# Performance work log

Measured on AMD Instinct MI355X. Metric: run time of the kernel, lower is better.

Reference implementation:

```python
import jax, jax.numpy as jnp
import numpy as np

B, T, D = 2, 4096, 1024
HD, HQ, KVH, W = 128, 8, 1, 1024   # head_dim, q_heads, kv_heads, window
HH, HG, K = 1536, 2048, 4          # hawk hidden, gmlp hidden, conv kernel
ALPHA_SCALE = float(np.log(8.0))   # alpha_log_scale (stored as log, used exp'd)


def setup_inputs() -> dict:
    key = jax.random.key(0)
    ks = jax.random.split(key, 16)
    n = lambda k, shape, std: jax.random.normal(k, shape, jnp.float32) * std
    return {
        'x': n(ks[0], (B, T, D), 1.0),
        'sn_g': jnp.ones((D,), jnp.float32),
        'q_w': n(ks[1], (HQ * HD, D), D ** -0.5),
        'kv_w': n(ks[2], (2 * KVH * HD, D), D ** -0.5),
        'ao_w': n(ks[3], (D, D), D ** -0.5),
        'sgn_g': jnp.ones((D,), jnp.float32),
        'sg_grow': n(ks[4], (2 * HG, D), D ** -0.5),
        'sg_shrink': n(ks[5], (D, HG), HG ** -0.5),
        'hn_g': jnp.ones((D,), jnp.float32),
        'h_in_w': n(ks[6], (2 * HH, D), D ** -0.5),
        'h_conv_w': n(ks[7], (HH, 1, K), K ** -0.5),
        'h_conv_b': jnp.zeros((HH,), jnp.float32),
        'h_gates_w': n(ks[8], (2 * HH, HH), HH ** -0.5),
        'h_gates_b': jnp.zeros((2 * HH,), jnp.float32),
        'h_forget': jnp.linspace(-4.323, -9.0, HH, dtype=jnp.float32),
        'h_out_w': n(ks[9], (D, HH), HH ** -0.5),
        'hgn_g': jnp.ones((D,), jnp.float32),
        'hg_grow': n(ks[10], (2 * HG, D), D ** -0.5),
        'hg_shrink': n(ks[11], (D, HG), HG ** -0.5),
    }


def rmsnorm(x, gamma):
    # original: gamma / dim**-0.5 * x / ||x||_2  (no eps)
    inv = jax.lax.rsqrt(jnp.sum(x * x, axis=-1, keepdims=True))
    return gamma * (x.shape[-1] ** 0.5) * x * inv


def rope(x, base=10000.0):
    # x: (B, T, H, HD); interleaved rotary over time axis 1
    t = x.shape[1]
    hd = x.shape[-1]
    inv = 1.0 / (base ** (jnp.arange(0, hd, 2, dtype=jnp.float32) / hd))
    ang = jnp.arange(t, dtype=jnp.float32)[:, None] * inv[None, :]  # (T, HD/2)
    cos = jnp.cos(ang)[None, :, None, :]
    sin = jnp.sin(ang)[None, :, None, :]
    x1, x2 = x[..., 0::2], x[..., 1::2]
    y1 = x1 * cos - x2 * sin
    y2 = x1 * sin + x2 * cos
    return jnp.stack([y1, y2], axis=-1).reshape(x.shape)


def sliding_mqa(x, q_w, kv_w, ao_w):
    # MQA with causal sliding window of W, computed in blocks of W
    q = (x @ q_w.T).reshape(B, T, HQ, HD)
    kv = (x @ kv_w.T).reshape(B, T, 2, KVH, HD)
    k = kv[:, :, 0, 0]  # (B, T, HD) since KVH == 1
    v = kv[:, :, 1, 0]
    q = rope(q)
    k = rope(k[:, :, None, :])[:, :, 0]
    nb = T // W
    qb = q.reshape(B, nb, W, HQ, HD)
    kb = k.reshape(B, nb, W, HD)
    vb = v.reshape(B, nb, W, HD)
    # prepend previous block (zeros for block 0)
    shift = lambda a: jnp.concatenate([jnp.zeros_like(a[:, :1]), a[:, :-1]], axis=1)
    k2 = jnp.concatenate([shift(kb), kb], axis=2)  # (B, nb, 2W, HD)
    v2 = jnp.concatenate([shift(vb), vb], axis=2)
    qi = jnp.arange(W)[:, None]
    kj = jnp.arange(2 * W)[None, :]
    base = (kj >= qi) & (kj <= qi + W)  # causal + window (i-j <= W)
    blk0 = base & (kj >= W)             # block 0 has no real previous block
    mask = jnp.where(jnp.arange(nb)[:, None, None] == 0, blk0[None], base[None])
    scores = jnp.einsum('bnqhd,bnkd->bhnqk', qb, k2) * (HD ** -0.5)
    scores = jnp.where(mask[None, None], scores, -jnp.inf)
    p = jax.nn.softmax(scores, axis=-1)
    o = jnp.einsum('bhnqk,bnkd->bnqhd', p, v2).reshape(B, T, HQ * HD)
    return o @ ao_w.T


def gated_mlp(x, grow_w, shrink_w):
    gate, h = jnp.split(x @ grow_w.T, 2, axis=-1)
    return (jax.nn.gelu(gate, approximate=False) * h) @ shrink_w.T


def hawk(x, in_w, conv_w, conv_b, gates_w, gates_b, forget_base, out_w):
    gate, u = jnp.split(x @ in_w.T, 2, axis=-1)  # (B, T, HH) each
    # depthwise causal conv1d (torch pads k-1 both sides then slices [:T])
    u_nch = jnp.transpose(u, (0, 2, 1))  # (B, HH, T)
    c = jax.lax.conv_general_dilated(
        u_nch, conv_w, window_strides=(1,), padding=[(K - 1, 0)],
        feature_group_count=HH, dimension_numbers=('NCH', 'OIH', 'NCH'))
    xc = jnp.transpose(c + conv_b[None, :, None], (0, 2, 1))  # (B, T, HH)
    fg, ig = jnp.split(xc @ gates_w.T + gates_b, 2, axis=-1)
    log_alpha = -np.exp(ALPHA_SCALE) * jax.nn.softplus(forget_base) * jax.nn.sigmoid(fg)
    alpha = jnp.exp(log_alpha)
    beta = jnp.sqrt(1.0 - alpha * alpha + 1e-6)
    xin = beta * jax.nn.sigmoid(ig) * xc
    # linear recurrence h_t = alpha_t * h_{t-1} + xin_t  via associative scan
    def combine(c1, c2):
        a1, x1 = c1
        a2, x2 = c2
        return a1 * a2, a2 * x1 + x2
    _, h = jax.lax.associative_scan(combine, (alpha, xin), axis=1)
    return (jax.nn.gelu(gate, approximate=False) * h) @ out_w.T


def reference(x, sn_g, q_w, kv_w, ao_w, sgn_g, sg_grow, sg_shrink,
              hn_g, h_in_w, h_conv_w, h_conv_b, h_gates_w, h_gates_b,
              h_forget, h_out_w, hgn_g, hg_grow, hg_shrink):
    x = x + sliding_mqa(rmsnorm(x, sn_g), q_w, kv_w, ao_w)
    x = x + gated_mlp(rmsnorm(x, sgn_g), sg_grow, sg_shrink)
    x = x + hawk(rmsnorm(x, hn_g), h_in_w, h_conv_w, h_conv_b,
                 h_gates_w, h_gates_b, h_forget, h_out_w)
    x = x + gated_mlp(rmsnorm(x, hgn_g), hg_grow, hg_shrink)
    return x
```

## Files before the change

### kernel.cpp

```cpp
#include <hip/hip_runtime.h>
#include <hip/hip_bf16.h>
#include <math.h>

#define B_  2
#define T_  4096
#define D_  1024
#define HD_ 128
#define HQ_ 8
#define W_  1024
#define HH_ 1536
#define HG_ 2048
#define KC_ 4

typedef float  f32x4  __attribute__((ext_vector_type(4)));
typedef float  f32x2  __attribute__((ext_vector_type(2)));
typedef __bf16 bf16x8 __attribute__((ext_vector_type(8)));
typedef unsigned short u16;
typedef unsigned short u16x2 __attribute__((ext_vector_type(2)));
typedef unsigned short u16x4 __attribute__((ext_vector_type(4)));
typedef unsigned short u16x8 __attribute__((ext_vector_type(8)));

__device__ __forceinline__ u16 f2bf(float f) {
    unsigned int u = __builtin_bit_cast(unsigned int, f);
    u += 0x7fffu + ((u >> 16) & 1u);
    return (u16)(u >> 16);
}
__device__ __forceinline__ float bf2f(u16 v) {
    unsigned int u = ((unsigned int)v) << 16;
    return __builtin_bit_cast(float, u);
}
__device__ __forceinline__ float gelu_exact(float x) {
    return 0.5f * x * (1.0f + erff(x * 0.70710678118654752f));
}
__device__ __forceinline__ float sigmoidf_(float x) {
    return 1.0f / (1.0f + expf(-x));
}

#define GLOAD16(gp, lp) __builtin_amdgcn_global_load_lds( \
    (const __attribute__((address_space(1))) void*)(gp),  \
    (__attribute__((address_space(3))) void*)(lp), 16, 0, 0)

__global__ void cvt_kernel(const float* __restrict__ src, u16* __restrict__ dst, long n)
{
    long i = ((long)blockIdx.x * blockDim.x + threadIdx.x) * 8;
    if (i >= n) return;
    f32x4 a = *(const f32x4*)(src + i);
    f32x4 b = *(const f32x4*)(src + i + 4);
    u16x4 ua, ub;
    ua.x = f2bf(a.x); ua.y = f2bf(a.y); ua.z = f2bf(a.z); ua.w = f2bf(a.w);
    ub.x = f2bf(b.x); ub.y = f2bf(b.y); ub.z = f2bf(b.z); ub.w = f2bf(b.w);
    *(u16x4*)(dst + i) = ua;
    *(u16x4*)(dst + i + 4) = ub;
}

template<int EPI, bool OBF>
__global__ __launch_bounds__(256)
void gemm_bf16_kernel(const u16* __restrict__ A, const u16* __restrict__ Bw,
                      const float* __restrict__ bias, const float* __restrict__ res,
                      const u16* gatebuf, void* outv,
                      int M, int N, int K)
{
    __shared__ u16 lA[2][128 * 32];
    __shared__ u16 lB[2][128 * 32];
    const int n0 = blockIdx.x * 128, m0 = blockIdx.y * 128;
    const int tid = threadIdx.x, w = tid >> 6, l = tid & 63;
    const int wr = w >> 1, wc = w & 1, lr = l & 15, lg = l >> 4;

    f32x4 acc[4][4];
#pragma unroll
    for (int i = 0; i < 4; i++)
#pragma unroll
        for (int j = 0; j < 4; j++) acc[i][j] = {0.f, 0.f, 0.f, 0.f};

    const int srow = w * 16 + (l >> 2);
    const int gslot = ((l & 3) - ((l >> 3) & 3)) & 3;
    const u16* gA = A + (long)(m0 + srow) * K + gslot * 8;
    const u16* gB = Bw + (long)(n0 + srow) * K + gslot * 8;
    const int lofs = w * 512 + l * 8;

#define STAGE_G(buf, kk)                                        \
    {                                                           \
        GLOAD16(gA + (kk),              &lA[buf][lofs]);        \
        GLOAD16(gA + (long)64 * K + (kk), &lA[buf][2048 + lofs]); \
        GLOAD16(gB + (kk),              &lB[buf][lofs]);        \
        GLOAD16(gB + (long)64 * K + (kk), &lB[buf][2048 + lofs]); \
    }

    STAGE_G(0, 0);
    __syncthreads();

    const int NT = K >> 5;
    const int swzr = (lr >> 1) & 3;
    for (int t = 0; t < NT; ++t) {
        const int cur = t & 1;
        if (t + 1 < NT) STAGE_G(cur ^ 1, (t + 1) << 5);
        bf16x8 af[4], bfr[4];
#pragma unroll
        for (int m = 0; m < 4; m++)
            af[m] = *(const bf16x8*)&lA[cur][(wr * 64 + m * 16 + lr) * 32 + (((lg + swzr) & 3) * 8)];
#pragma unroll
        for (int n = 0; n < 4; n++)
            bfr[n] = *(const bf16x8*)&lB[cur][(wc * 64 + n * 16 + lr) * 32 + (((lg + swzr) & 3) * 8)];
#pragma unroll
        for (int m = 0; m < 4; m++)
#pragma unroll
            for (int n = 0; n < 4; n++)
                acc[m][n] = __builtin_amdgcn_mfma_f32_16x16x32_bf16(af[m], bfr[n], acc[m][n], 0, 0, 0);
        __syncthreads();
    }
#undef STAGE_G

#pragma unroll
    for (int m = 0; m < 4; m++)
#pragma unroll
        for (int n = 0; n < 4; n++) {
            const int col = n0 + wc * 64 + n * 16 + lr;
            const float bv = (EPI == 1) ? bias[col] : 0.f;
#pragma unroll
            for (int r = 0; r < 4; r++) {
                const int row = m0 + wr * 64 + m * 16 + lg * 4 + r;
                const long idx = (long)row * N + col;
                float v = acc[m][n][r] + bv;
                if (EPI == 2) v += res[idx];
                if (EPI == 3) v = gelu_exact(bf2f(gatebuf[idx])) * v;
                if (OBF) ((u16*)outv)[idx] = f2bf(v);
                else     ((float*)outv)[idx] = v;
            }
        }
}

__global__ __launch_bounds__(256)
void rmsnorm_kernel(const float* __restrict__ x, const float* __restrict__ g,
                    u16* __restrict__ out)
{
    const long row = blockIdx.x;
    const int tid = threadIdx.x;
    const float* xp = x + row * D_;
    f32x4 v = *(const f32x4*)(xp + tid * 4);
    float ss = v.x * v.x + v.y * v.y + v.z * v.z + v.w * v.w;
#pragma unroll
    for (int o = 1; o < 64; o <<= 1) ss += __shfl_xor(ss, o);
    __shared__ float ps[4];
    if ((tid & 63) == 0) ps[tid >> 6] = ss;
    __syncthreads();
    float tot = ps[0] + ps[1] + ps[2] + ps[3];
    float inv = rsqrtf(tot) * 32.0f;
    f32x4 gv = *(const f32x4*)(g + tid * 4);
    u16x4 o4;
    o4.x = f2bf(gv.x * v.x * inv); o4.y = f2bf(gv.y * v.y * inv);
    o4.z = f2bf(gv.z * v.z * inv); o4.w = f2bf(gv.w * v.w * inv);
    *(u16x4*)(out + row * D_ + tid * 4) = o4;
}

__global__ void rope_bf16_kernel(const float* __restrict__ q, const float* __restrict__ kv,
                                 u16* __restrict__ qb, u16* __restrict__ kb)
{
    const long NQ = (long)B_ * T_ * HQ_ * 64;
    const long NK = (long)B_ * T_ * 64;
    long idx = (long)blockIdx.x * blockDim.x + threadIdx.x;
    if (idx >= NQ + NK) return;
    int i; long t; const float* src; u16* dst;
    if (idx < NQ) {
        i = idx & 63;
        long bth = idx >> 6;
        t = (bth / HQ_) % T_;
        src = q + bth * HD_ + 2 * i;
        dst = qb + bth * HD_ + 2 * i;
    } else {
        long k = idx - NQ;
        i = k & 63;
        long bt = k >> 6;
        t = bt % T_;
        src = kv + bt * (2 * HD_) + 2 * i;
        dst = kb + bt * HD_ + 2 * i;
    }
    float freq = exp2f(-(float)i * 0.20762050593046014f);
    float ang = (float)t * freq;
    float sn, cs;
    sincosf(ang, &sn, &cs);
    f32x2 xv = *(const f32x2*)src;
    u16x2 yv;
    yv.x = f2bf(xv.x * cs - xv.y * sn);
    yv.y = f2bf(xv.x * sn + xv.y * cs);
    *(u16x2*)dst = yv;
}

__global__ __launch_bounds__(256)
void vtrans_kernel(const float* __restrict__ kv, u16* __restrict__ vt)
{
    __shared__ float tile[64][65];
    const int t0 = blockIdx.x * 64, d0 = blockIdx.y * 64, b = blockIdx.z;
    const int tid = threadIdx.x;
    {
        const int tl = tid & 63, dg = tid >> 6;
        const float* vp = kv + (((long)b * T_ + t0 + tl) * 2 + 1) * HD_ + d0 + dg * 16;
#pragma unroll
        for (int j = 0; j < 4; j++) {
            f32x4 v = *(const f32x4*)(vp + j * 4);
            tile[dg * 16 + j * 4 + 0][tl] = v.x;
            tile[dg * 16 + j * 4 + 1][tl] = v.y;
            tile[dg * 16 + j * 4 + 2][tl] = v.z;
            tile[dg * 16 + j * 4 + 3][tl] = v.w;
        }
    }
    __syncthreads();
    {
        const int dl = tid >> 2, tg = (tid & 3) * 16;
        u16x8 a, c;
#pragma unroll
        for (int j = 0; j < 8; j++) a[j] = f2bf(tile[dl][tg + j]);
#pragma unroll
        for (int j = 0; j < 8; j++) c[j] = f2bf(tile[dl][tg + 8 + j]);
        u16* dst = vt + ((long)b * HD_ + d0 + dl) * T_ + t0 + tg;
        *(u16x8*)dst = a;
        *(u16x8*)(dst + 8) = c;
    }
}

#define PLD 72

__global__ __launch_bounds__(256)
void attn_mfma3_kernel(const u16* __restrict__ qb, const u16* __restrict__ kb,
                       const u16* __restrict__ vt, u16* __restrict__ o)
{
    __shared__ u16 Ksh[2][64 * 128];
    __shared__ u16 Vsh[2][128 * 64];
    __shared__ u16 Psh[4 * 16 * PLD];

    const int qt = blockIdx.x, h = blockIdx.y, b = blockIdx.z;
    const int q0 = qt * 64;
    const int tid = threadIdx.x;
    const int w = tid >> 6, l = tid & 63;
    const int lr = l & 15, lg = l >> 4;

    bf16x8 qfr[4];
    {
        const u16* qp = qb + (((long)b * T_ + q0 + w * 16 + lr) * HQ_ + h) * HD_;
#pragma unroll
        for (int kt = 0; kt < 4; kt++)
            qfr[kt] = *(const bf16x8*)(qp + kt * 32 + lg * 8);
    }

    int oK[4], oV[4];
#pragma unroll
    for (int i = 0; i < 4; i++) {
        int krow = w * 16 + i * 4 + (l >> 4);
        int kc8 = (l & 15) ^ (krow & 7);
        oK[i] = krow * 128 + kc8 * 8;
        int vrow = w * 32 + i * 8 + (l >> 3);
        int vc8 = (l & 7) ^ (vrow & 7);
        oV[i] = vrow * T_ + vc8 * 8;
    }
    const u16* kbase = kb + (long)b * T_ * HD_;
    const u16* vbase = vt + (long)b * HD_ * T_;

    f32x4 oacc[8];
#pragma unroll
    for (int dt = 0; dt < 8; dt++) oacc[dt] = {0.f, 0.f, 0.f, 0.f};
    float mrun[4], srun[4];
#pragma unroll
    for (int r = 0; r < 4; r++) { mrun[r] = -1e30f; srun[r] = 0.f; }

    const int kt_lo = (q0 >= W_) ? (q0 - W_) : 0;
    const int nt = ((q0 - kt_lo) >> 6) + 1;
    const int sw = lr & 7;
    const float scale = 0.08838834764831845f;

#pragma unroll
    for (int i = 0; i < 4; i++) {
        GLOAD16(kbase + (long)kt_lo * HD_ + oK[i], &Ksh[0][w * 2048 + i * 512]);
        GLOAD16(vbase + kt_lo + oV[i], &Vsh[0][w * 2048 + i * 512]);
    }

    for (int t = 0; t < nt; ++t) {
        const int kt0 = kt_lo + t * 64;
        const int cur = t & 1;
        if (t + 1 < nt) {
            const int ktn = kt0 + 64;
#pragma unroll
            for (int i = 0; i < 4; i++) {
                GLOAD16(kbase + (long)ktn * HD_ + oK[i], &Ksh[cur ^ 1][w * 2048 + i * 512]);
                GLOAD16(vbase + ktn + oV[i], &Vsh[cur ^ 1][w * 2048 + i * 512]);
            }
            asm volatile("s_waitcnt vmcnt(8)" ::: "memory");
        } else {
            asm volatile("s_waitcnt vmcnt(0)" ::: "memory");
        }
        __builtin_amdgcn_s_barrier();
        __builtin_amdgcn_sched_barrier(0);

        const u16* Kc = Ksh[cur];
        const u16* Vc = Vsh[cur];

        f32x4 s[4];
        __builtin_amdgcn_s_setprio(1);
#pragma unroll
        for (int ct = 0; ct < 4; ct++) {
            s[ct] = {0.f, 0.f, 0.f, 0.f};
#pragma unroll
            for (int kt = 0; kt < 4; kt++) {
                bf16x8 kf = *(const bf16x8*)&Kc[(ct * 16 + lr) * 128 + (((kt * 4 + lg) ^ sw) * 8)];
                s[ct] = __builtin_amdgcn_mfma_f32_16x16x32_bf16(qfr[kt], kf, s[ct], 0, 0, 0);
            }
        }
        __builtin_amdgcn_s_setprio(0);

        float tmax[4] = {-3e38f, -3e38f, -3e38f, -3e38f};
        if (kt0 == q0) {
#pragma unroll
            for (int ct = 0; ct < 4; ct++) {
                const int kpos = kt0 + ct * 16 + lr;
#pragma unroll
                for (int r = 0; r < 4; r++) {
                    const int qpos = q0 + w * 16 + lg * 4 + r;
                    float v = s[ct][r] * scale;
                    v = (kpos <= qpos) ? v : -3e38f;
                    s[ct][r] = v;
                    tmax[r] = fmaxf(tmax[r], v);
                }
            }
        } else if (kt0 == q0 - W_) {
#pragma unroll
            for (int ct = 0; ct < 4; ct++) {
                const int kpos = kt0 + ct * 16 + lr;
#pragma unroll
                for (int r = 0; r < 4; r++) {
                    const int qpos = q0 + w * 16 + lg * 4 + r;
                    float v = s[ct][r] * scale;
                    v = (kpos + W_ >= qpos) ? v : -3e38f;
                    s[ct][r] = v;
                    tmax[r] = fmaxf(tmax[r], v);
                }
            }
        } else {
#pragma unroll
            for (int ct = 0; ct < 4; ct++)
#pragma unroll
                for (int r = 0; r < 4; r++) {
                    float v = s[ct][r] * scale;
                    s[ct][r] = v;
                    tmax[r] = fmaxf(tmax[r], v);
                }
        }
#pragma unroll
        for (int r = 0; r < 4; r++)
#pragma unroll
            for (int msk = 1; msk < 16; msk <<= 1)
                tmax[r] = fmaxf(tmax[r], __shfl_xor(tmax[r], msk));

        bool defer = (tmax[0] <= mrun[0] + 8.f) && (tmax[1] <= mrun[1] + 8.f) &&
                     (tmax[2] <= mrun[2] + 8.f) && (tmax[3] <= mrun[3] + 8.f);
        if (!__all(defer)) {
            float frv[4];
#pragma unroll
            for (int r = 0; r < 4; r++) {
                float mnew = fmaxf(mrun[r], tmax[r]);
                frv[r] = __expf(mrun[r] - mnew);
                mrun[r] = mnew;
                srun[r] *= frv[r];
            }
#pragma unroll
            for (int dt = 0; dt < 8; dt++) {
                oacc[dt][0] *= frv[0]; oacc[dt][1] *= frv[1];
                oacc[dt][2] *= frv[2]; oacc[dt][3] *= frv[3];
            }
        }

        u16* pw = &Psh[w * 16 * PLD];
        float psum[4] = {0.f, 0.f, 0.f, 0.f};
#pragma unroll
        for (int ct = 0; ct < 4; ct++)
#pragma unroll
            for (int r = 0; r < 4; r++) {
                float p = __expf(s[ct][r] - mrun[r]);
                psum[r] += p;
                pw[(lg * 4 + r) * PLD + ct * 16 + lr] = f2bf(p);
            }
#pragma unroll
        for (int r = 0; r < 4; r++) {
#pragma unroll
            for (int msk = 1; msk < 16; msk <<= 1)
                psum[r] += __shfl_xor(psum[r], msk);
            srun[r] += psum[r];
        }

        asm volatile("s_waitcnt lgkmcnt(0)" ::: "memory");
        bf16x8 pa0 = *(const bf16x8*)&pw[lr * PLD + lg * 8];
        bf16x8 pa1 = *(const bf16x8*)&pw[lr * PLD + 32 + lg * 8];
        __builtin_amdgcn_s_setprio(1);
#pragma unroll
        for (int dt = 0; dt < 8; dt++) {
            bf16x8 vf0 = *(const bf16x8*)&Vc[(dt * 16 + lr) * 64 + ((lg ^ sw) * 8)];
            bf16x8 vf1 = *(const bf16x8*)&Vc[(dt * 16 + lr) * 64 + (((4 + lg) ^ sw) * 8)];
            oacc[dt] = __builtin_amdgcn_mfma_f32_16x16x32_bf16(pa0, vf0, oacc[dt], 0, 0, 0);
            oacc[dt] = __builtin_amdgcn_mfma_f32_16x16x32_bf16(pa1, vf1, oacc[dt], 0, 0, 0);
        }
        __builtin_amdgcn_s_setprio(0);
        __syncthreads();
    }

#pragma unroll
    for (int r = 0; r < 4; r++) {
        const int qpos = q0 + w * 16 + lg * 4 + r;
        float inv = 1.f / srun[r];
        u16* op = o + ((long)b * T_ + qpos) * (HQ_ * HD_) + h * HD_;
#pragma unroll
        for (int dt = 0; dt < 8; dt++)
            op[dt * 16 + lr] = f2bf(oacc[dt][r] * inv);
    }
}

__global__ void conv_kernel(const u16* __restrict__ u, const float* __restrict__ w,
                            const float* __restrict__ bias, u16* __restrict__ xc)
{
    long idx = (long)blockIdx.x * blockDim.x + threadIdx.x;
    if (idx >= (long)B_ * T_ * HH_) return;
    int ch = (int)(idx % HH_);
    long row = idx / HH_;
    int t = (int)(row % T_);
    float acc = bias[ch];
#pragma unroll
    for (int k = 0; k < KC_; k++) {
        int ts = t - 3 + k;
        if (ts >= 0) acc += bf2f(u[(row - t + ts) * HH_ + ch]) * w[ch * KC_ + k];
    }
    xc[idx] = f2bf(acc);
}

#define CS_ 64
#define NC_ (T_ / CS_)

__device__ __forceinline__ void alpha_xin(const u16 fg, const u16 ig, const u16 xc,
                                          float sp, float& a, float& xin)
{
    a = expf(-8.0f * sp * sigmoidf_(bf2f(fg)));
    xin = sqrtf(1.f - a * a + 1e-6f) * sigmoidf_(bf2f(ig)) * bf2f(xc);
}

__global__ void scan1_kernel(const u16* __restrict__ fg, const u16* __restrict__ ig,
                             const u16* __restrict__ xc, const float* __restrict__ fb,
                             float* __restrict__ P, float* __restrict__ L)
{
    long idx = (long)blockIdx.x * blockDim.x + threadIdx.x;
    if (idx >= (long)B_ * NC_ * HH_) return;
    int ch = (int)(idx % HH_);
    int chunk = (int)((idx / HH_) % NC_);
    int b = (int)(idx / ((long)HH_ * NC_));
    long base = ((long)b * T_ + chunk * CS_) * HH_ + ch;
    float f = fb[ch];
    float sp = (f > 20.f) ? f : log1pf(expf(f));
    float p = 1.f, lacc = 0.f;
    for (int i = 0; i < CS_; i++) {
        long o = base + (long)i * HH_;
        float a, xin;
        alpha_xin(fg[o], ig[o], xc[o], sp, a, xin);
        lacc = a * lacc + xin;
        p *= a;
    }
    P[idx] = p; L[idx] = lacc;
}
__global__ void scan2_kernel(const float* __restrict__ P, const float* __restrict__ L,
                             float* __restrict__ I)
{
    long idx = (long)blockIdx.x * blockDim.x + threadIdx.x;
    if (idx >= (long)B_ * HH_) return;
    int ch = (int)(idx % HH_);
    int b = (int)(idx / HH_);
    float init = 0.f;
    for (int c = 0; c < NC_; c++) {
        long o = ((long)b * NC_ + c) * HH_ + ch;
        I[o] = init;
        init = P[o] * init + L[o];
    }
}
__global__ void scan3_kernel(const u16* __restrict__ fg, const u16* __restrict__ ig,
                             const u16* __restrict__ xc, const float* __restrict__ fb,
                             const float* __restrict__ I, const u16* __restrict__ gate,
                             u16* __restrict__ glu)
{
    long idx = (long)blockIdx.x * blockDim.x + threadIdx.x;
    if (idx >= (long)B_ * NC_ * HH_) return;
    int ch = (int)(idx % HH_);
    int chunk = (int)((idx / HH_) % NC_);
    int b = (int)(idx / ((long)HH_ * NC_));
    long base = ((long)b * T_ + chunk * CS_) * HH_ + ch;
    float f = fb[ch];
    float sp = (f > 20.f) ? f : log1pf(expf(f));
    float h = I[idx];
    for (int i = 0; i < CS_; i++) {
        long o = base + (long)i * HH_;
        float a, xin;
        alpha_xin(fg[o], ig[o], xc[o], sp, a, xin);
        h = a * h + xin;
        glu[o] = f2bf(gelu_exact(bf2f(gate[o])) * h);
    }
}

static inline long cdivl(long a, long b) { return (a + b - 1) / b; }

extern "C" void kernel_launch(void* const* d_in, const int* in_sizes, int n_in,
                              void* d_out, int out_size, void* d_ws, size_t ws_size,
                              hipStream_t stream)
{
    const float* x_in   = (const float*)d_in[0];
    const float* sn_g   = (const float*)d_in[1];
    const float* q_w    = (const float*)d_in[2];
    const float* kv_w   = (const float*)d_in[3];
    const float* ao_w   = (const float*)d_in[4];
    const float* sgn_g  = (const float*)d_in[5];
    const float* sg_grow   = (const float*)d_in[6];
    const float* sg_shrink = (const float*)d_in[7];
    const float* hn_g   = (const float*)d_in[8];
    const float* h_in_w = (const float*)d_in[9];
    const float* h_conv_w = (const float*)d_in[10];
    const float* h_conv_b = (const float*)d_in[11];
    const float* h_gates_w = (const float*)d_in[12];
    const float* h_gates_b = (const float*)d_in[13];
    const float* h_forget  = (const float*)d_in[14];
    const float* h_out_w   = (const float*)d_in[15];
    const float* hgn_g  = (const float*)d_in[16];
    const float* hg_grow   = (const float*)d_in[17];
    const float* hg_shrink = (const float*)d_in[18];
    float* out = (float*)d_out;

    char* wsb = (char*)d_ws;
    u16* Wq  = (u16*)wsb;
    u16* Wkv = Wq  + 1048576;
    u16* Wao = Wkv + 262144;
    u16* Wsg = Wao + 1048576;
    u16* Wss = Wsg + 4194304;
    u16* Whi = Wss + 2097152;
    u16* Whg = Whi + 3145728;
    u16* Who = Whg + 4718592;
    u16* Wgg = Who + 1572864;
    u16* Wgs = Wgg + 4194304;
    char* ab = wsb + 48758784;
    u16*   XN   = (u16*)(ab + 0);
    char*  S2   = ab + 16777216;
    char*  S3   = ab + 50331648;
    char*  S4   = ab + 75497472;
    char*  S5   = ab + 100663296;
    char*  S6   = ab + 125829120;
    float* PB   = (float*)(ab + 150994944);
    float* LB   = (float*)(ab + 151781376);
    float* IB   = (float*)(ab + 152567808);

    const long M = (long)B_ * T_;
    dim3 blk(256);
    const float* NULF = nullptr;
    const u16*   NULB = nullptr;

    {
        const float* srcs[10] = {q_w, kv_w, ao_w, sg_grow, sg_shrink,
                                 h_in_w, h_gates_w, h_out_w, hg_grow, hg_shrink};
        u16* dsts[10] = {Wq, Wkv, Wao, Wsg, Wss, Whi, Whg, Who, Wgg, Wgs};
        long ns[10] = {1048576, 262144, 1048576, 4194304, 2097152,
                       3145728, 4718592, 1572864, 4194304, 2097152};
        for (int i = 0; i < 10; i++)
            cvt_kernel<<<dim3(cdivl(ns[i] / 8, 256)), blk, 0, stream>>>(srcs[i], dsts[i], ns[i]);
    }

    {
        float* Q  = (float*)S2;
        float* KV = (float*)S3;
        u16*   Kb = (u16*)(S3 + 8388608);
        u16*   Vt = (u16*)(S3 + 10485760);
        u16*   Qb = (u16*)S4;
        u16*   AT = (u16*)S5;
        rmsnorm_kernel<<<dim3(M), blk, 0, stream>>>(x_in, sn_g, XN);
        gemm_bf16_kernel<0,false><<<dim3(8, 64), blk, 0, stream>>>(XN, Wq, NULF, NULF, NULB, Q, M, 1024, 1024);
        gemm_bf16_kernel<0,false><<<dim3(2, 64), blk, 0, stream>>>(XN, Wkv, NULF, NULF, NULB, KV, M, 256, 1024);
        rope_bf16_kernel<<<dim3(cdivl((long)B_ * T_ * (HQ_ + 1) * 64, 256)), blk, 0, stream>>>(Q, KV, Qb, Kb);
        vtrans_kernel<<<dim3(T_ / 64, 2, B_), blk, 0, stream>>>(KV, Vt);
        attn_mfma3_kernel<<<dim3(T_ / 64, HQ_, B_), blk, 0, stream>>>(Qb, Kb, Vt, AT);
        gemm_bf16_kernel<2,false><<<dim3(8, 64), blk, 0, stream>>>(AT, Wao, NULF, x_in, NULB, out, M, 1024, 1024);
    }

    {
        u16* GATE = (u16*)S2;
        rmsnorm_kernel<<<dim3(M), blk, 0, stream>>>(out, sgn_g, XN);
        gemm_bf16_kernel<0,true><<<dim3(16, 64), blk, 0, stream>>>(XN, Wsg, NULF, NULF, NULB, GATE, M, 2048, 1024);
        gemm_bf16_kernel<3,true><<<dim3(16, 64), blk, 0, stream>>>(XN, Wsg + (size_t)2048 * 1024, NULF, NULF, GATE, GATE, M, 2048, 1024);
        gemm_bf16_kernel<2,false><<<dim3(8, 64), blk, 0, stream>>>(GATE, Wss, NULF, out, NULB, out, M, 1024, 2048);
    }

    {
        u16* GATEH = (u16*)S2;
        u16* U     = (u16*)S3;
        u16* XC    = (u16*)S4;
        u16* FG    = (u16*)S5;
        u16* IG    = (u16*)S6;
        rmsnorm_kernel<<<dim3(M), blk, 0, stream>>>(out, hn_g, XN);
        gemm_bf16_kernel<0,true><<<dim3(12, 64), blk, 0, stream>>>(XN, Whi, NULF, NULF, NULB, GATEH, M, 1536, 1024);
        gemm_bf16_kernel<0,true><<<dim3(12, 64), blk, 0, stream>>>(XN, Whi + (size_t)1536 * 1024, NULF, NULF, NULB, U, M, 1536, 1024);
        conv_kernel<<<dim3(cdivl(M * HH_, 256)), blk, 0, stream>>>(U, h_conv_w, h_conv_b, XC);
        gemm_bf16_kernel<1,true><<<dim3(12, 64), blk, 0, stream>>>(XC, Whg, h_gates_b, NULF, NULB, FG, M, 1536, 1536);
        gemm_bf16_kernel<1,true><<<dim3(12, 64), blk, 0, stream>>>(XC, Whg + (size_t)1536 * 1536, h_gates_b + 1536, NULF, NULB, IG, M, 1536, 1536);
        scan1_kernel<<<dim3(cdivl((long)B_ * NC_ * HH_, 256)), blk, 0, stream>>>(FG, IG, XC, h_forget, PB, LB);
        scan2_kernel<<<dim3(cdivl((long)B_ * HH_, 256)), blk, 0, stream>>>(PB, LB, IB);
        scan3_kernel<<<dim3(cdivl((long)B_ * NC_ * HH_, 256)), blk, 0, stream>>>(FG, IG, XC, h_forget, IB, GATEH, U);
        gemm_bf16_kernel<2,false><<<dim3(8, 64), blk, 0, stream>>>(U, Who, NULF, out, NULB, out, M, 1024, 1536);
    }

    {
        u16* GLU = (u16*)S2;
        rmsnorm_kernel<<<dim3(M), blk, 0, stream>>>(out, hgn_g, XN);
        gemm_bf16_kernel<0,true><<<dim3(16, 64), blk, 0, stream>>>(XN, Wgg, NULF, NULF, NULB, GLU, M, 2048, 1024);
        gemm_bf16_kernel<3,true><<<dim3(16, 64), blk, 0, stream>>>(XN, Wgg + (size_t)2048 * 1024, NULF, NULF, GLU, GLU, M, 2048, 1024);
        gemm_bf16_kernel<2,false><<<dim3(8, 64), blk, 0, stream>>>(GLU, Wgs, NULF, out, NULB, out, M, 1024, 2048);
    }
}
```

Measured before the change: 1.086 ms.

## Triple-buffer GEMM LDS pipeline and merge weight conversions into one launch

```diff
diff --git a/kernel.cpp b/kernel.cpp
--- a/kernel.cpp
+++ b/kernel.cpp
@@ -40,17 +40,29 @@
     (const __attribute__((address_space(1))) void*)(gp),  \
     (__attribute__((address_space(3))) void*)(lp), 16, 0, 0)
 
-__global__ void cvt_kernel(const float* __restrict__ src, u16* __restrict__ dst, long n)
-{
-    long i = ((long)blockIdx.x * blockDim.x + threadIdx.x) * 8;
-    if (i >= n) return;
-    f32x4 a = *(const f32x4*)(src + i);
-    f32x4 b = *(const f32x4*)(src + i + 4);
+struct CvtArgs {
+    const float* src[10];
+    u16* dst[10];
+    long cum[11];
+};
+__global__ __launch_bounds__(256)
+void cvt_all_kernel(CvtArgs a)
+{
+    long i = ((long)blockIdx.x * 256 + threadIdx.x) * 8;
+    if (i >= a.cum[10]) return;
+    int seg = 0;
+#pragma unroll
+    for (int s = 1; s < 10; s++) if (i >= a.cum[s]) seg = s;
+    long off = i - a.cum[seg];
+    const float* src = a.src[seg];
+    u16* dst = a.dst[seg];
+    f32x4 x = *(const f32x4*)(src + off);
+    f32x4 y = *(const f32x4*)(src + off + 4);
     u16x4 ua, ub;
-    ua.x = f2bf(a.x); ua.y = f2bf(a.y); ua.z = f2bf(a.z); ua.w = f2bf(a.w);
-    ub.x = f2bf(b.x); ub.y = f2bf(b.y); ub.z = f2bf(b.z); ub.w = f2bf(b.w);
-    *(u16x4*)(dst + i) = ua;
-    *(u16x4*)(dst + i + 4) = ub;
+    ua.x = f2bf(x.x); ua.y = f2bf(x.y); ua.z = f2bf(x.z); ua.w = f2bf(x.w);
+    ub.x = f2bf(y.x); ub.y = f2bf(y.y); ub.z = f2bf(y.z); ub.w = f2bf(y.w);
+    *(u16x4*)(dst + off) = ua;
+    *(u16x4*)(dst + off + 4) = ub;
 }
 
 template<int EPI, bool OBF>
@@ -60,8 +72,8 @@
                       const u16* gatebuf, void* outv,
                       int M, int N, int K)
 {
-    __shared__ u16 lA[2][128 * 32];
-    __shared__ u16 lB[2][128 * 32];
+    __shared__ u16 lA[3][128 * 32];
+    __shared__ u16 lB[3][128 * 32];
     const int n0 = blockIdx.x * 128, m0 = blockIdx.y * 128;
     const int tid = threadIdx.x, w = tid >> 6, l = tid & 63;
     const int wr = w >> 1, wc = w & 1, lr = l & 15, lg = l >> 4;
@@ -78,22 +90,29 @@
     const u16* gB = Bw + (long)(n0 + srow) * K + gslot * 8;
     const int lofs = w * 512 + l * 8;
 
-#define STAGE_G(buf, kk)                                        \
-    {                                                           \
-        GLOAD16(gA + (kk),              &lA[buf][lofs]);        \
+#define STAGE_G(buf, kk)                                          \
+    {                                                             \
+        GLOAD16(gA + (kk),                &lA[buf][lofs]);        \
         GLOAD16(gA + (long)64 * K + (kk), &lA[buf][2048 + lofs]); \
-        GLOAD16(gB + (kk),              &lB[buf][lofs]);        \
+        GLOAD16(gB + (kk),                &lB[buf][lofs]);        \
         GLOAD16(gB + (long)64 * K + (kk), &lB[buf][2048 + lofs]); \
     }
 
+    const int NT = K >> 5;
     STAGE_G(0, 0);
-    __syncthreads();
-
-    const int NT = K >> 5;
+    STAGE_G(1, 32);
+
     const int swzr = (lr >> 1) & 3;
+    int cur = 0;
     for (int t = 0; t < NT; ++t) {
-        const int cur = t & 1;
-        if (t + 1 < NT) STAGE_G(cur ^ 1, (t + 1) << 5);
+        if (t == NT - 1) { asm volatile("s_waitcnt vmcnt(0)" ::: "memory"); }
+        else             { asm volatile("s_waitcnt vmcnt(4)" ::: "memory"); }
+        __builtin_amdgcn_s_barrier();
+        __builtin_amdgcn_sched_barrier(0);
+        if (t + 2 < NT) {
+            int nb = cur + 2; if (nb >= 3) nb -= 3;
+            STAGE_G(nb, (t + 2) << 5);
+        }
         bf16x8 af[4], bfr[4];
 #pragma unroll
         for (int m = 0; m < 4; m++)
@@ -101,12 +120,14 @@
 #pragma unroll
         for (int n = 0; n < 4; n++)
             bfr[n] = *(const bf16x8*)&lB[cur][(wc * 64 + n * 16 + lr) * 32 + (((lg + swzr) & 3) * 8)];
+        __builtin_amdgcn_s_setprio(1);
 #pragma unroll
         for (int m = 0; m < 4; m++)
 #pragma unroll
             for (int n = 0; n < 4; n++)
                 acc[m][n] = __builtin_amdgcn_mfma_f32_16x16x32_bf16(af[m], bfr[n], acc[m][n], 0, 0, 0);
-        __syncthreads();
+        __builtin_amdgcn_s_setprio(0);
+        cur++; if (cur == 3) cur = 0;
     }
 #undef STAGE_G
 
@@ -551,13 +572,18 @@
     const u16*   NULB = nullptr;
 
     {
+        CvtArgs ca;
         const float* srcs[10] = {q_w, kv_w, ao_w, sg_grow, sg_shrink,
                                  h_in_w, h_gates_w, h_out_w, hg_grow, hg_shrink};
         u16* dsts[10] = {Wq, Wkv, Wao, Wsg, Wss, Whi, Whg, Who, Wgg, Wgs};
         long ns[10] = {1048576, 262144, 1048576, 4194304, 2097152,
                        3145728, 4718592, 1572864, 4194304, 2097152};
-        for (int i = 0; i < 10; i++)
-            cvt_kernel<<<dim3(cdivl(ns[i] / 8, 256)), blk, 0, stream>>>(srcs[i], dsts[i], ns[i]);
+        long cum = 0;
+        for (int i = 0; i < 10; i++) {
+            ca.src[i] = srcs[i]; ca.dst[i] = dsts[i]; ca.cum[i] = cum; cum += ns[i];
+        }
+        ca.cum[10] = cum;
+        cvt_all_kernel<<<dim3(cdivl(cum / 8, 256)), blk, 0, stream>>>(ca);
     }
 
     {
```

Measured after the change: 1.075 ms. About the same (-1.0%).
